# Performance work log

Measured on AMD Instinct MI355X. Metric: run time of the kernel, lower is better.

## Reference

```python
import jax, jax.numpy as jnp
import numpy as np
from jax import lax

ROPE_THETA = 10000.0


def rotate_half(x):
    d = x.shape[-1] // 2
    return jnp.concatenate([-x[..., d:], x[..., :d]], axis=-1)


def segsum(x):
    # x: (..., l) -> (..., l, l) lower-triangular segment sums (off-tri = -inf)
    T = x.shape[-1]
    cs = jnp.cumsum(x, axis=-1)
    d = cs[..., :, None] - cs[..., None, :]
    mask = jnp.tril(jnp.ones((T, T), dtype=bool))
    return jnp.where(mask, d, -jnp.inf)


def setup_inputs() -> dict:
    key = jax.random.key(0)
    ks = jax.random.split(key, 8)
    B, L, D, H = 2, 8192, 1024, 16
    P = D // H  # head_dim == state_dim
    hidden_states = jax.random.normal(ks[0], (B, L, D), dtype=jnp.float32)
    # rotary embeddings over head_dim
    inv_freq = 1.0 / (ROPE_THETA ** (np.arange(0, P, 2, dtype=np.float32) / P))
    pos = np.arange(L, dtype=np.float32)
    freqs = pos[:, None] * inv_freq[None, :]            # (L, P/2)
    emb = np.concatenate([freqs, freqs], axis=-1)       # (L, P)
    cos = jnp.asarray(np.broadcast_to(np.cos(emb), (B, L, P)).copy())
    sin = jnp.asarray(np.broadcast_to(np.sin(emb), (B, L, P)).copy())
    s = 1.0 / np.sqrt(D)
    Wc = jax.random.normal(ks[1], (D, D), dtype=jnp.float32) * s
    Wb = jax.random.normal(ks[2], (D, D), dtype=jnp.float32) * s
    Wx = jax.random.normal(ks[3], (D, D), dtype=jnp.float32) * s
    Wdt = jax.random.normal(ks[4], (D, H), dtype=jnp.float32) * s
    Wout = jax.random.normal(ks[5], (D, D), dtype=jnp.float32) * s
    # A must be negative for a stable decaying SSM (Mamba2 convention A = -exp(A_log))
    A = -(0.5 + jax.random.uniform(ks[6], (H,), dtype=jnp.float32))
    return {"hidden_states": hidden_states, "cos": cos, "sin": sin,
            "Wc": Wc, "Wb": Wb, "Wdt": Wdt, "Wx": Wx, "Wout": Wout,
            "A": A, "chunk_size": 256}


def reference(hidden_states, cos, sin, Wc, Wb, Wdt, Wx, Wout, A, chunk_size):
    B, L, D = hidden_states.shape
    H = A.shape[0]
    P = D // H
    nc = L // chunk_size
    cl = chunk_size

    c = (hidden_states @ Wc).reshape(B, L, H, P)
    b = (hidden_states @ Wb).reshape(B, L, H, P)
    x = (hidden_states @ Wx).reshape(B, L, H, P)
    dt = jax.nn.softplus(hidden_states @ Wdt)  # (B, L, H), dt_softplus=True

    # rotary on C and B (unsqueeze_dim=2)
    cosu, sinu = cos[:, :, None, :], sin[:, :, None, :]
    c = c * cosu + rotate_half(c) * sinu
    b = b * cosu + rotate_half(b) * sinu

    # chunked SSD (mamba_chunk_scan_combined)
    cr = c.reshape(B, nc, cl, H, P)
    br = b.reshape(B, nc, cl, H, P)
    xdt = (x * dt[..., None]).reshape(B, nc, cl, H, P)
    dA = (dt * A[None, None, :]).reshape(B, nc, cl, H)
    dAc = jnp.transpose(dA, (0, 3, 1, 2))            # (B, H, nc, cl)
    Acum = jnp.cumsum(dAc, axis=-1)                  # (B, H, nc, cl)

    # intra-chunk (diagonal) term
    Lmask = jnp.exp(segsum(dAc))                     # (B, H, nc, cl, cl)
    Y_diag = jnp.einsum('bclhn,bcshn,bhcls,bcshp->bclhp', cr, br, Lmask, xdt)

    # per-chunk states
    decay_states = jnp.exp(Acum[..., -1:] - Acum)    # (B, H, nc, cl)
    states = jnp.einsum('bclhn,bhcl,bclhp->bchpn', br, decay_states, xdt)
    chunk_decay = jnp.exp(Acum[..., -1])             # (B, H, nc)

    def step(h, inp):
        s, dec = inp                                 # (B,H,P,N), (B,H)
        h_new = h * dec[..., None, None] + s
        return h_new, h                              # emit state BEFORE this chunk

    states_c = jnp.moveaxis(states, 1, 0)            # (nc, B, H, P, N)
    dec_c = jnp.moveaxis(chunk_decay, 2, 0)          # (nc, B, H)
    h0 = jnp.zeros((B, H, P, P), dtype=hidden_states.dtype)
    final_state, prev_states = lax.scan(step, h0, (states_c, dec_c))
    prev_states = jnp.moveaxis(prev_states, 0, 1)    # (B, nc, H, P, N)

    # inter-chunk (off-diagonal) term
    state_decay_out = jnp.exp(Acum)                  # (B, H, nc, cl)
    Y_off = jnp.einsum('bclhn,bchpn,bhcl->bclhp', cr, prev_states, state_decay_out)

    y = (Y_diag + Y_off).reshape(B, L, D)
    out = y @ Wout
    return out, final_state
```

## Files before the change

### kernel.cpp

```cpp
#include <hip/hip_runtime.h>
#include <hip/hip_bf16.h>

typedef unsigned short u16;

#define Bb 2
#define Ll 8192
#define Dd 1024
#define Hh 16
#define Pp 64
#define CLc 256
#define NCc 32
#define Mm 16384
#define DD2 ((size_t)Dd*Dd)
#define WDTSZ ((size_t)256*1024)

typedef __attribute__((ext_vector_type(8))) short short8b;
typedef __attribute__((ext_vector_type(4))) float f32x4v;

__device__ __forceinline__ float bf2f(u16 u){
    return __uint_as_float(((unsigned int)u) << 16);
}
__device__ __forceinline__ u16 f2bf(float f){
    unsigned int i = __float_as_uint(f);
    unsigned int r = (i + 0x7FFFu + ((i >> 16) & 1u)) >> 16;
    return (u16)r;
}

template<int DT>
__device__ __forceinline__ void ld8(const void* p, size_t i, float* o){
    if (DT){
        const u16* q = (const u16*)p + i;
        ushort4 a0 = *(const ushort4*)q;
        ushort4 a1 = *(const ushort4*)(q + 4);
        o[0]=bf2f(a0.x); o[1]=bf2f(a0.y); o[2]=bf2f(a0.z); o[3]=bf2f(a0.w);
        o[4]=bf2f(a1.x); o[5]=bf2f(a1.y); o[6]=bf2f(a1.z); o[7]=bf2f(a1.w);
    } else {
        const float* q = (const float*)p + i;
        float4 a0 = *(const float4*)q;
        float4 a1 = *(const float4*)(q + 4);
        o[0]=a0.x; o[1]=a0.y; o[2]=a0.z; o[3]=a0.w;
        o[4]=a1.x; o[5]=a1.y; o[6]=a1.z; o[7]=a1.w;
    }
}
__device__ __forceinline__ float ldf(const void* p, size_t i, int dtf){
    return dtf ? bf2f(((const u16*)p)[i]) : ((const float*)p)[i];
}

typedef __attribute__((address_space(3))) void lds_t;
typedef __attribute__((address_space(1))) const void gm_t;
__device__ __forceinline__ void gload16(const void* g, void* l){
    __builtin_amdgcn_global_load_lds((gm_t*)g, (lds_t*)l, 16, 0, 0);
}

__device__ __forceinline__ void fence_barrier(){
    asm volatile("" ::: "memory");
    __builtin_amdgcn_s_barrier();
    asm volatile("" ::: "memory");
}

__global__ void sniff_kernel(const unsigned int* __restrict__ cosw, int* __restrict__ flag){
    if (threadIdx.x == 0 && blockIdx.x == 0)
        *flag = (cosw[0] == 0x3F800000u) ? 0 : 1;
}

__global__ __launch_bounds__(256) void cospack_kernel(
    const void* __restrict__ cosb, const void* __restrict__ sinb,
    float* __restrict__ cp, const int* __restrict__ flag)
{
    const int dtf = *flag;
    int i = blockIdx.x*256 + threadIdx.x;
    int tok = i >> 6, c = i & 63;
    float v = (c < 32) ? ldf(cosb, (size_t)tok*64 + c,        dtf)
                       : ldf(sinb, (size_t)tok*64 + (c - 32), dtf);
    cp[i] = v;
}

__global__ __launch_bounds__(256) void cvt_kernel(
    const void* __restrict__ in, u16* __restrict__ out, const int* __restrict__ flag)
{
    if (*flag == 1) return;
    size_t i = ((size_t)blockIdx.x*256 + threadIdx.x) * 8;
    float v[8];
    ld8<0>(in, i, v);
    ushort4 o0, o1;
    o0.x=f2bf(v[0]); o0.y=f2bf(v[1]); o0.z=f2bf(v[2]); o0.w=f2bf(v[3]);
    o1.x=f2bf(v[4]); o1.y=f2bf(v[5]); o1.z=f2bf(v[6]); o1.w=f2bf(v[7]);
    *(ushort4*)(out + i)     = o0;
    *(ushort4*)(out + i + 4) = o1;
}

__global__ __launch_bounds__(256) void wtrans_kernel(
    const void* __restrict__ W0, const void* __restrict__ W1,
    const void* __restrict__ W2, const void* __restrict__ W3,
    u16* __restrict__ out, const int* __restrict__ flag)
{
    const int dtf = *flag;
    const int z = blockIdx.z;
    const void* W = (z==0) ? W0 : (z==1) ? W1 : (z==2) ? W2 : W3;
    u16* Whi = out + (size_t)z*DD2 + (z==3 ? WDTSZ : 0);
    u16* Wlo = out + (size_t)4*DD2 + WDTSZ;
    __shared__ u16 th[64][65];
    __shared__ u16 tlo[64][65];
    const int t = threadIdx.x;
    const int r = t >> 2, cq = (t & 3)*16;
    size_t base = ((size_t)blockIdx.y*64 + r)*1024 + (size_t)blockIdx.x*64 + cq;
    float v[8];
#pragma unroll
    for (int half = 0; half < 2; half++){
        if (dtf) ld8<1>(W, base + half*8, v); else ld8<0>(W, base + half*8, v);
#pragma unroll
        for (int j = 0; j < 8; j++){
            u16 hi = f2bf(v[j]);
            th[r][cq + half*8 + j]  = hi;
            tlo[r][cq + half*8 + j] = f2bf(v[j] - bf2f(hi));
        }
    }
    __syncthreads();
    size_t ob = ((size_t)blockIdx.x*64 + r)*1024 + (size_t)blockIdx.y*64 + cq;
#pragma unroll
    for (int j = 0; j < 16; j++)
        Whi[ob + j] = th[cq + j][r];
    if (z == 3){
#pragma unroll
        for (int j = 0; j < 16; j++)
            Wlo[ob + j] = tlo[cq + j][r];
    }
}

__global__ __launch_bounds__(256) void wdtrep_kernel(
    const void* __restrict__ Wdt, u16* __restrict__ wdt, const int* __restrict__ flag)
{
    const int dtf = *flag;
    int i = blockIdx.x*256 + threadIdx.x;
    int r = i >> 10, k = i & 1023;
    wdt[i] = f2bf(ldf(Wdt, (size_t)k*16 + (r & 15), dtf));
}

template<int DTC, int ACC, int FUSE>
__global__ __launch_bounds__(512) void gemm_mfma(
    const u16* __restrict__ Abf, const void* __restrict__ Araw,
    const u16* __restrict__ Bt, void* __restrict__ C,
    int M, int N, int K, const int* __restrict__ flag, int want,
    const float* __restrict__ cp, float* __restrict__ dtb)
{
    const int dtf = *flag;
    if (want >= 0 && dtf != want) return;
    const u16* A = (FUSE && dtf) ? (const u16*)Araw : Abf;
    __shared__ __align__(128) u16 As[4][256*32];
    __shared__ __align__(128) u16 Bs[4][256*32];
    const int t    = threadIdx.x;
    const int wave = t >> 6;
    const int lane = t & 63;

    const int nbn = N >> 8;
    const int nbm = M >> 8;
    int wg = blockIdx.x, nwg = gridDim.x;
    int bm, bn;
    if ((nwg & 7) == 0 && (nbm & 7) == 0){
        const int x   = wg & 7;
        const int loc = wg >> 3;
        const int rpx = nbm >> 3;
        const int bmL = loc % rpx;
        bn = loc / rpx;
        bm = x*rpx + bmL;
    } else {
        bm = wg / nbn; bn = wg % nbn;
    }

    const int ldrow = wave*16 + (lane >> 2);
    const int ldk   = (lane & 3)*8;
    const u16* Ag0 = A  + (size_t)(bm*256 + ldrow)*K + ldk;
    const u16* Ag1 = Ag0 + (size_t)128*K;
    const u16* Bg0 = Bt + (size_t)(bn*256 + ldrow)*K + ldk;
    const u16* Bg1 = Bg0 + (size_t)128*K;
    const int o0 = (wave*16)*32;
    const int o1 = (128 + wave*16)*32;

    const int wr = wave >> 2, wc = wave & 3;
    const int fr = lane & 15;
    const int fk = (lane >> 4)*8;

    f32x4v acc[8][4] = {};

    const int steps = K >> 5;
#pragma unroll
    for (int s = 0; s < 2; s++){
        gload16(Ag0 + s*32, &As[s][o0]);
        gload16(Ag1 + s*32, &As[s][o1]);
        gload16(Bg0 + s*32, &Bs[s][o0]);
        gload16(Bg1 + s*32, &Bs[s][o1]);
    }

    for (int ts = 0; ts < steps; ++ts){
        if (ts + 2 < steps){
            const int sb = (ts + 2) & 3;
            const int ko = (ts + 2)*32;
            gload16(Ag0 + ko, &As[sb][o0]);
            gload16(Ag1 + ko, &As[sb][o1]);
            gload16(Bg0 + ko, &Bs[sb][o0]);
            gload16(Bg1 + ko, &Bs[sb][o1]);
            asm volatile("s_waitcnt vmcnt(8)" ::: "memory");
        } else if (ts + 1 < steps){
            asm volatile("s_waitcnt vmcnt(4)" ::: "memory");
        } else {
            asm volatile("s_waitcnt vmcnt(0)" ::: "memory");
        }
        fence_barrier();
        const int cb = ts & 3;
        const u16* a_rd = &As[cb][(wr*128 + fr)*32 + fk];
        const u16* b_rd = &Bs[cb][(wc*64 + fr)*32 + fk];
        short8b af[8], bfv[4];
#pragma unroll
        for (int i = 0; i < 8; i++)
            af[i]  = *(const short8b*)(a_rd + i*16*32);
#pragma unroll
        for (int i = 0; i < 4; i++)
            bfv[i] = *(const short8b*)(b_rd + i*16*32);
#pragma unroll
        for (int mi = 0; mi < 8; mi++)
#pragma unroll
            for (int ni = 0; ni < 4; ni++)
                acc[mi][ni] = __builtin_amdgcn_mfma_f32_16x16x32_bf16(
                    af[mi], bfv[ni], acc[mi][ni], 0, 0, 0);
    }

    const int crow = (lane >> 4)*4;
    const int ccol = lane & 15;

    if (FUSE && bn == nbn - 1){
        if (wc == 0){
#pragma unroll
            for (int mi = 0; mi < 8; mi++){
#pragma unroll
                for (int r = 0; r < 4; r++){
                    size_t row = (size_t)bm*256 + wr*128 + mi*16 + crow + r;
                    float v = acc[mi][0][r];
                    float sp = (v > 20.f) ? v : log1pf(__expf(v));
                    dtb[row*16 + ccol] = sp;
                }
            }
        }
        return;
    }

    const int bufid = FUSE ? (bn >> 2) : 0;
    const int bnl   = FUSE ? (bn & 3) : bn;
    u16* Cf = FUSE ? ((u16*)C + (size_t)bufid*((size_t)Mm*Dd)) : (u16*)C;
    const size_t Nout = FUSE ? (size_t)Dd : (size_t)N;

    if (FUSE && bufid < 2){
#pragma unroll
        for (int mi = 0; mi < 8; mi++){
#pragma unroll
            for (int r = 0; r < 4; r++){
                size_t row = (size_t)bm*256 + wr*128 + mi*16 + crow + r;
                const float* cpr = cp + (size_t)(row & (Ll-1))*64;
                float cs0 = cpr[ccol],      cs1 = cpr[ccol + 16];
                float sn0 = cpr[32 + ccol], sn1 = cpr[48 + ccol];
                float a0 = acc[mi][0][r], a1 = acc[mi][1][r];
                float a2 = acc[mi][2][r], a3 = acc[mi][3][r];
                acc[mi][0][r] = a0*cs0 - a2*sn0;
                acc[mi][2][r] = a2*cs0 + a0*sn0;
                acc[mi][1][r] = a1*cs1 - a3*sn1;
                acc[mi][3][r] = a3*cs1 + a1*sn1;
            }
        }
    }

#pragma unroll
    for (int mi = 0; mi < 8; mi++){
#pragma unroll
        for (int ni = 0; ni < 4; ni++){
            size_t col = (size_t)bnl*256 + wc*64 + ni*16 + ccol;
#pragma unroll
            for (int r = 0; r < 4; r++){
                size_t row = (size_t)bm*256 + wr*128 + mi*16 + crow + r;
                float v = acc[mi][ni][r];
                if (DTC){
                    Cf[row*Nout + col] = f2bf(v);
                } else {
                    float* p = (float*)C + row*Nout + col;
                    *p = ACC ? (*p + v) : v;
                }
            }
        }
    }
}

__global__ __launch_bounds__(512) void chunk_kernel(
    const u16* __restrict__ cr, u16* brY, const u16* __restrict__ xd,
    float* __restrict__ Acum, float* __restrict__ states,
    const float* __restrict__ dtb, const void* __restrict__ Aarr,
    const int* __restrict__ flag)
{
    __shared__ u16 brs[256*72];
    __shared__ u16 brTs[64*264];
    __shared__ u16 xdsT[64*264];
    __shared__ u16 plds[8][32*72];
    __shared__ float acs[256];
    __shared__ float wexp[256];
    const int dtf = *flag;
    const int g = blockIdx.x;
    const int h = g & 15, c = (g >> 4) & 31, b = g >> 9;
    const int t = threadIdx.x;
    const int w = t >> 6, lane = t & 63;
    const size_t tokbase = (size_t)b*Ll + (size_t)c*CLc;
    float* Acw = Acum + ((size_t)(b*Hh + h)*NCc + c)*CLc;

    if (t < 256)
        acs[t] = dtb[(tokbase + t)*Hh + h] * ldf(Aarr, h, dtf);
    __syncthreads();
    for (int off = 1; off < 256; off <<= 1){
        float add = (t < 256 && t >= off) ? acs[t - off] : 0.f;
        __syncthreads();
        if (t < 256) acs[t] += add;
        __syncthreads();
    }
    const float a_last = acs[255];
    if (t < 256){
        wexp[t] = __expf(fminf(a_last - acs[t], 0.f));
        Acw[t] = acs[t];
    }
    __syncthreads();

#pragma unroll
    for (int i = 0; i < 4; i++){
        int f8 = i*512 + t;
        int l  = f8 >> 3;
        int n8 = (f8 & 7)*8;
        size_t goff = (tokbase + l)*Dd + h*Pp + n8;
        ushort4 a0 = *(const ushort4*)&brY[goff];
        ushort4 a1 = *(const ushort4*)&brY[goff + 4];
        *(ushort4*)&brs[l*72 + n8]     = a0;
        *(ushort4*)&brs[l*72 + n8 + 4] = a1;
        float wl = wexp[l];
        u16 bv[8] = {(u16)a0.x,(u16)a0.y,(u16)a0.z,(u16)a0.w,
                     (u16)a1.x,(u16)a1.y,(u16)a1.z,(u16)a1.w};
#pragma unroll
        for (int j = 0; j < 8; j++)
            brTs[(n8 + j)*264 + l] = f2bf(wl * bf2f(bv[j]));
        float dl = dtb[(tokbase + l)*Hh + h];
        ushort4 x0 = *(const ushort4*)&xd[goff];
        ushort4 x1 = *(const ushort4*)&xd[goff + 4];
        u16 xv[8] = {(u16)x0.x,(u16)x0.y,(u16)x0.z,(u16)x0.w,
                     (u16)x1.x,(u16)x1.y,(u16)x1.z,(u16)x1.w};
#pragma unroll
        for (int j = 0; j < 8; j++)
            xdsT[(n8 + j)*264 + l] = f2bf(bf2f(xv[j]) * dl);
    }
    __syncthreads();

    const int fr = lane & 15;
    const int kb = (lane >> 4)*8;

    {
        int ks0 = 0;
        for (int ks = 0; ks < 8; ks++){
            if (a_last - acs[ks*32 + 31] >= -30.f){ ks0 = ks; break; }
        }
        const int pi  = w >> 1;
        const int ni0 = (w & 1)*2;
        f32x4v sacc[2] = {};
        const int pr = pi*16 + fr;
        for (int ks = ks0; ks < 8; ks++){
            short8b afr = *(const short8b*)&xdsT[pr*264 + ks*32 + kb];
#pragma unroll
            for (int q = 0; q < 2; q++){
                short8b bfr = *(const short8b*)&brTs[((ni0+q)*16 + fr)*264 + ks*32 + kb];
                sacc[q] = __builtin_amdgcn_mfma_f32_16x16x32_bf16(afr, bfr, sacc[q], 0, 0, 0);
            }
        }
        float* st = states + ((size_t)((b*NCc + c)*Hh) + h)*4096;
        const int prow = pi*16 + (lane >> 4)*4;
#pragma unroll
        for (int q = 0; q < 2; q++)
#pragma unroll
            for (int r = 0; r < 4; r++)
                st[(prow + r)*64 + (ni0+q)*16 + fr] = sacc[q][r];
    }

    {
        short8b crf[2][2];
#pragma unroll
        for (int mi = 0; mi < 2; mi++)
#pragma unroll
            for (int ks = 0; ks < 2; ks++)
                crf[mi][ks] = *(const short8b*)&cr[(tokbase + w*32 + mi*16 + fr)*Dd + h*Pp + ks*32 + kb];

        float al[2][4];
#pragma unroll
        for (int mi = 0; mi < 2; mi++)
#pragma unroll
            for (int r = 0; r < 4; r++)
                al[mi][r] = acs[w*32 + mi*16 + (lane >> 4)*4 + r];

        f32x4v yacc[2][4] = {};
        u16* pw = &plds[w][0];
        const float a_hi = acs[w*32];

        for (int cb = w >> 1; cb >= 0; --cb){
            if (a_hi - acs[cb*64 + 63] < -30.f) break;
#pragma unroll
            for (int mi = 0; mi < 2; mi++){
#pragma unroll
                for (int ni = 0; ni < 4; ni++){
                    f32x4v s4 = {};
#pragma unroll
                    for (int ks = 0; ks < 2; ks++){
                        short8b bfr = *(const short8b*)&brs[(cb*64 + ni*16 + fr)*72 + ks*32 + kb];
                        s4 = __builtin_amdgcn_mfma_f32_16x16x32_bf16(crf[mi][ks], bfr, s4, 0, 0, 0);
                    }
                    const int s_idx = cb*64 + ni*16 + fr;
                    const float a_s = acs[s_idx];
                    const int lrow0 = w*32 + mi*16 + (lane >> 4)*4;
#pragma unroll
                    for (int r = 0; r < 4; r++){
                        float wgt = __expf(fminf(al[mi][r] - a_s, 0.f));
                        float pv  = (s_idx <= lrow0 + r) ? wgt * s4[r] : 0.f;
                        pw[(mi*16 + (lane >> 4)*4 + r)*72 + ni*16 + fr] = f2bf(pv);
                    }
                }
            }
            asm volatile("s_waitcnt lgkmcnt(0)" ::: "memory");
#pragma unroll
            for (int ks = 0; ks < 2; ks++){
                short8b paf[2];
#pragma unroll
                for (int mi = 0; mi < 2; mi++)
                    paf[mi] = *(const short8b*)&pw[(mi*16 + fr)*72 + ks*32 + kb];
#pragma unroll
                for (int pi = 0; pi < 4; pi++){
                    short8b xbf = *(const short8b*)&xdsT[(pi*16 + fr)*264 + cb*64 + ks*32 + kb];
#pragma unroll
                    for (int mi = 0; mi < 2; mi++)
                        yacc[mi][pi] = __builtin_amdgcn_mfma_f32_16x16x32_bf16(paf[mi], xbf, yacc[mi][pi], 0, 0, 0);
                }
            }
        }
#pragma unroll
        for (int mi = 0; mi < 2; mi++){
            const int lrow = w*32 + mi*16 + (lane >> 4)*4;
#pragma unroll
            for (int r = 0; r < 4; r++){
                u16* yp = brY + (tokbase + lrow + r)*Dd + h*Pp + fr;
#pragma unroll
                for (int pi = 0; pi < 4; pi++)
                    yp[pi*16] = f2bf(yacc[mi][pi][r]);
            }
        }
    }
}

__global__ __launch_bounds__(256) void scan_kernel(
    float* st, const float* __restrict__ Acum, void* d_out, const int* __restrict__ flag)
{
    const int dtf = *flag;
    const int g = blockIdx.x;
    const int seg = g & 15;
    const int bh = g >> 4;
    const int h = bh & 15, b = bh >> 4;
    const int e = seg*256 + threadIdx.x;
    const float* Ac = Acum + (size_t)(b*Hh + h)*NCc*CLc;
    float hst = 0.f;
    for (int c = 0; c < NCc; c++){
        float dec = __expf(fminf(Ac[c*CLc + 255], 0.f));
        size_t off = ((size_t)((b*NCc + c)*Hh) + h)*4096 + e;
        float s_val = st[off];
        st[off] = hst;
        hst = hst*dec + s_val;
    }
    size_t fi = (size_t)Mm*Dd + (size_t)(b*Hh + h)*4096 + e;
    if (dtf) ((u16*)d_out)[fi] = f2bf(hst);
    else     ((float*)d_out)[fi] = hst;
}

__global__ __launch_bounds__(256) void yoff_kernel(
    const u16* __restrict__ cr, const float* __restrict__ prev,
    const float* __restrict__ Acum, u16* y)
{
    __shared__ u16 pvb[64*72];
    __shared__ float acs[256];
    const int g = blockIdx.x;
    const int h = g & 15, c = (g >> 4) & 31, b = g >> 9;
    const int t = threadIdx.x;
    const int wv = t >> 6, lane = t & 63;
    const size_t tokbase = (size_t)b*Ll + (size_t)c*CLc;
    const float* pv = prev + ((size_t)((b*NCc + c)*Hh) + h)*4096;
    const float* Ac = Acum + ((size_t)(b*Hh + h)*NCc + c)*CLc;
    acs[t] = Ac[t];
#pragma unroll
    for (int i = 0; i < 16; i++){
        int f = i*256 + t;
        int p = f >> 6, n = f & 63;
        pvb[p*72 + n] = f2bf(pv[f]);
    }
    __syncthreads();

    const int fr = lane & 15;
    const int kb = (lane >> 4)*8;

    short8b crf[4][2];
#pragma unroll
    for (int mi = 0; mi < 4; mi++)
#pragma unroll
        for (int ks = 0; ks < 2; ks++)
            crf[mi][ks] = *(const short8b*)&cr[(tokbase + wv*64 + mi*16 + fr)*Dd + h*Pp + ks*32 + kb];

    f32x4v yacc[4][4] = {};
#pragma unroll
    for (int ks = 0; ks < 2; ks++){
        short8b pbf[4];
#pragma unroll
        for (int pi = 0; pi < 4; pi++)
            pbf[pi] = *(const short8b*)&pvb[(pi*16 + fr)*72 + ks*32 + kb];
#pragma unroll
        for (int mi = 0; mi < 4; mi++)
#pragma unroll
            for (int pi = 0; pi < 4; pi++)
                yacc[mi][pi] = __builtin_amdgcn_mfma_f32_16x16x32_bf16(
                    crf[mi][ks], pbf[pi], yacc[mi][pi], 0, 0, 0);
    }

    const int crw = (lane >> 4)*4;
#pragma unroll
    for (int mi = 0; mi < 4; mi++){
        const int lrow = wv*64 + mi*16 + crw;
#pragma unroll
        for (int r = 0; r < 4; r++){
            float el = __expf(fminf(acs[lrow + r], 0.f));
            u16* yp = y + (tokbase + lrow + r)*Dd + h*Pp + fr;
#pragma unroll
            for (int pi = 0; pi < 4; pi++){
                float cur = bf2f(yp[pi*16]);
                yp[pi*16] = f2bf(cur + el*yacc[mi][pi][r]);
            }
        }
    }
}

__global__ __launch_bounds__(256) void zero_out_kernel(void* o, long long n, const int* flag)
{
    long long i = (long long)blockIdx.x*256 + threadIdx.x;
    if (i < n){
        if (*flag) ((u16*)o)[i] = 0;
        else       ((float*)o)[i] = 0.f;
    }
}

extern "C" void kernel_launch(void* const* d_in, const int* in_sizes, int n_in,
                              void* d_out, int out_size, void* d_ws, size_t ws_size,
                              hipStream_t stream)
{
    const void* hs   = d_in[0];
    const void* cosb = d_in[1];
    const void* sinb = d_in[2];
    const void* Wc   = d_in[3];
    const void* Wb   = d_in[4];
    const void* Wdt  = d_in[5];
    const void* Wx   = d_in[6];
    const void* Wout = d_in[7];
    const void* Aarr = d_in[8];

    int*  flag  = (int*)d_ws;
    char* wbase = (char*)d_ws + 1024;

    const size_t NEED = 1024
                      + (size_t)3*Mm*Dd*2
                      + (size_t)Mm*Hh*4
                      + (size_t)Bb*Hh*Ll*4
                      + (size_t)Bb*NCc*Hh*4096*4
                      + (size_t)Mm*Dd*2
                      + ((size_t)5*DD2 + WDTSZ)*2
                      + (size_t)Ll*64*4;

    sniff_kernel<<<1, 64, 0, stream>>>((const unsigned int*)cosb, flag);

    if (ws_size < NEED){
        long long n = (long long)out_size;
        zero_out_kernel<<<(unsigned)((n + 255)/256), 256, 0, stream>>>(d_out, n, flag);
        return;
    }

    u16*   c_buf  = (u16*)wbase;
    u16*   b_buf  = c_buf + (size_t)Mm*Dd;
    u16*   x_buf  = b_buf + (size_t)Mm*Dd;
    float* dt_buf = (float*)(x_buf + (size_t)Mm*Dd);
    float* acum   = dt_buf + (size_t)Mm*Hh;
    float* states = acum + (size_t)Bb*Hh*Ll;
    u16*   hs_bf  = (u16*)(states + (size_t)Bb*NCc*Hh*4096);
    u16*   wt     = hs_bf + (size_t)Mm*Dd;
    float* cp     = (float*)(wt + (size_t)5*DD2 + WDTSZ);

    cvt_kernel<<<(Mm*Dd)/(256*8), 256, 0, stream>>>(hs, hs_bf, flag);
    wtrans_kernel<<<dim3(16,16,4), 256, 0, stream>>>(Wc, Wb, Wx, Wout, wt, flag);
    wdtrep_kernel<<<(256*1024)/256, 256, 0, stream>>>(Wdt, wt + 3*DD2, flag);
    cospack_kernel<<<(Ll*64)/256, 256, 0, stream>>>(cosb, sinb, cp, flag);

    gemm_mfma<1,0,1><<<(Mm/256)*(3328/256), 512, 0, stream>>>(
        hs_bf, hs, wt, c_buf, Mm, 3328, Dd, flag, -1, cp, dt_buf);

    chunk_kernel<<<Bb*NCc*Hh, 512, 0, stream>>>(c_buf, b_buf, x_buf, acum, states, dt_buf, Aarr, flag);
    scan_kernel<<<Bb*Hh*16, 256, 0, stream>>>(states, acum, d_out, flag);
    yoff_kernel<<<Bb*NCc*Hh, 256, 0, stream>>>(c_buf, states, acum, b_buf);

    const int NWG = (Mm/256)*(Dd/256);
    u16* woutT = wt + 3*DD2 + WDTSZ;
    u16* woutL = wt + 4*DD2 + WDTSZ;
    gemm_mfma<1,0,0><<<NWG, 512, 0, stream>>>(b_buf, nullptr, woutT, d_out, Mm, Dd, Dd, flag, 1, nullptr, nullptr);
    gemm_mfma<0,0,0><<<NWG, 512, 0, stream>>>(b_buf, nullptr, woutT, d_out, Mm, Dd, Dd, flag, 0, nullptr, nullptr);
    gemm_mfma<0,1,0><<<NWG, 512, 0, stream>>>(b_buf, nullptr, woutL, d_out, Mm, Dd, Dd, flag, 0, nullptr, nullptr);
}
```

Baseline: 478.7 us.

## Shrink GEMM tiles to 128x128 with 256 threads and double buffering

Replaces the 256x256-tile, 512-thread GEMM with a 128x128-tile, 256-thread version. The four-stage LDS ring with explicit vmcnt waits becomes a two-buffer scheme synchronised by __syncthreads. The fused projection GEMM now uses N=3200, with the dt columns in a single 128-wide tile. Smaller tiles give more workgroups and less LDS per block, in exchange for lower operand reuse and shallower prefetch that exposes more global-load latency.

```diff
diff --git a/kernel.cpp b/kernel.cpp
--- a/kernel.cpp
+++ b/kernel.cpp
@@ -52,12 +52,6 @@
     __builtin_amdgcn_global_load_lds((gm_t*)g, (lds_t*)l, 16, 0, 0);
 }
 
-__device__ __forceinline__ void fence_barrier(){
-    asm volatile("" ::: "memory");
-    __builtin_amdgcn_s_barrier();
-    asm volatile("" ::: "memory");
-}
-
 __global__ void sniff_kernel(const unsigned int* __restrict__ cosw, int* __restrict__ flag){
     if (threadIdx.x == 0 && blockIdx.x == 0)
         *flag = (cosw[0] == 0x3F800000u) ? 0 : 1;
@@ -137,7 +131,7 @@
 }
 
 template<int DTC, int ACC, int FUSE>
-__global__ __launch_bounds__(512) void gemm_mfma(
+__global__ __launch_bounds__(256) void gemm_mfma(
     const u16* __restrict__ Abf, const void* __restrict__ Araw,
     const u16* __restrict__ Bt, void* __restrict__ C,
     int M, int N, int K, const int* __restrict__ flag, int want,
@@ -146,14 +140,14 @@
     const int dtf = *flag;
     if (want >= 0 && dtf != want) return;
     const u16* A = (FUSE && dtf) ? (const u16*)Araw : Abf;
-    __shared__ __align__(128) u16 As[4][256*32];
-    __shared__ __align__(128) u16 Bs[4][256*32];
+    __shared__ __align__(128) u16 As[2][128*32];
+    __shared__ __align__(128) u16 Bs[2][128*32];
     const int t    = threadIdx.x;
     const int wave = t >> 6;
     const int lane = t & 63;
 
-    const int nbn = N >> 8;
-    const int nbm = M >> 8;
+    const int nbn = N >> 7;
+    const int nbm = M >> 7;
     int wg = blockIdx.x, nwg = gridDim.x;
     int bm, bn;
     if ((nwg & 7) == 0 && (nbm & 7) == 0){
@@ -169,59 +163,51 @@
 
     const int ldrow = wave*16 + (lane >> 2);
     const int ldk   = (lane & 3)*8;
-    const u16* Ag0 = A  + (size_t)(bm*256 + ldrow)*K + ldk;
-    const u16* Ag1 = Ag0 + (size_t)128*K;
-    const u16* Bg0 = Bt + (size_t)(bn*256 + ldrow)*K + ldk;
-    const u16* Bg1 = Bg0 + (size_t)128*K;
+    const u16* Ag0 = A  + (size_t)(bm*128 + ldrow)*K + ldk;
+    const u16* Ag1 = Ag0 + (size_t)64*K;
+    const u16* Bg0 = Bt + (size_t)(bn*128 + ldrow)*K + ldk;
+    const u16* Bg1 = Bg0 + (size_t)64*K;
     const int o0 = (wave*16)*32;
-    const int o1 = (128 + wave*16)*32;
-
-    const int wr = wave >> 2, wc = wave & 3;
+    const int o1 = (64 + wave*16)*32;
+
+    const int wr = wave >> 1, wc = wave & 1;
     const int fr = lane & 15;
     const int fk = (lane >> 4)*8;
 
-    f32x4v acc[8][4] = {};
+    f32x4v acc[4][4] = {};
 
     const int steps = K >> 5;
-#pragma unroll
-    for (int s = 0; s < 2; s++){
-        gload16(Ag0 + s*32, &As[s][o0]);
-        gload16(Ag1 + s*32, &As[s][o1]);
-        gload16(Bg0 + s*32, &Bs[s][o0]);
-        gload16(Bg1 + s*32, &Bs[s][o1]);
-    }
+    gload16(Ag0, &As[0][o0]);
+    gload16(Ag1, &As[0][o1]);
+    gload16(Bg0, &Bs[0][o0]);
+    gload16(Bg1, &Bs[0][o1]);
+    __syncthreads();
 
     for (int ts = 0; ts < steps; ++ts){
-        if (ts + 2 < steps){
-            const int sb = (ts + 2) & 3;
-            const int ko = (ts + 2)*32;
-            gload16(Ag0 + ko, &As[sb][o0]);
-            gload16(Ag1 + ko, &As[sb][o1]);
-            gload16(Bg0 + ko, &Bs[sb][o0]);
-            gload16(Bg1 + ko, &Bs[sb][o1]);
-            asm volatile("s_waitcnt vmcnt(8)" ::: "memory");
-        } else if (ts + 1 < steps){
-            asm volatile("s_waitcnt vmcnt(4)" ::: "memory");
-        } else {
-            asm volatile("s_waitcnt vmcnt(0)" ::: "memory");
-        }
-        fence_barrier();
-        const int cb = ts & 3;
-        const u16* a_rd = &As[cb][(wr*128 + fr)*32 + fk];
-        const u16* b_rd = &Bs[cb][(wc*64 + fr)*32 + fk];
-        short8b af[8], bfv[4];
-#pragma unroll
-        for (int i = 0; i < 8; i++)
+        const int cur = ts & 1;
+        if (ts + 1 < steps){
+            const int nb = cur ^ 1;
+            const int ko = (ts + 1)*32;
+            gload16(Ag0 + ko, &As[nb][o0]);
+            gload16(Ag1 + ko, &As[nb][o1]);
+            gload16(Bg0 + ko, &Bs[nb][o0]);
+            gload16(Bg1 + ko, &Bs[nb][o1]);
+        }
+        const u16* a_rd = &As[cur][(wr*64 + fr)*32 + fk];
+        const u16* b_rd = &Bs[cur][(wc*64 + fr)*32 + fk];
+        short8b af[4], bfv[4];
+#pragma unroll
+        for (int i = 0; i < 4; i++){
             af[i]  = *(const short8b*)(a_rd + i*16*32);
-#pragma unroll
-        for (int i = 0; i < 4; i++)
             bfv[i] = *(const short8b*)(b_rd + i*16*32);
-#pragma unroll
-        for (int mi = 0; mi < 8; mi++)
+        }
+#pragma unroll
+        for (int mi = 0; mi < 4; mi++)
 #pragma unroll
             for (int ni = 0; ni < 4; ni++)
                 acc[mi][ni] = __builtin_amdgcn_mfma_f32_16x16x32_bf16(
                     af[mi], bfv[ni], acc[mi][ni], 0, 0, 0);
+        __syncthreads();
     }
 
     const int crow = (lane >> 4)*4;
@@ -230,10 +216,10 @@
     if (FUSE && bn == nbn - 1){
         if (wc == 0){
 #pragma unroll
-            for (int mi = 0; mi < 8; mi++){
+            for (int mi = 0; mi < 4; mi++){
 #pragma unroll
                 for (int r = 0; r < 4; r++){
-                    size_t row = (size_t)bm*256 + wr*128 + mi*16 + crow + r;
+                    size_t row = (size_t)bm*128 + wr*64 + mi*16 + crow + r;
                     float v = acc[mi][0][r];
                     float sp = (v > 20.f) ? v : log1pf(__expf(v));
                     dtb[row*16 + ccol] = sp;
@@ -243,17 +229,17 @@
         return;
     }
 
-    const int bufid = FUSE ? (bn >> 2) : 0;
-    const int bnl   = FUSE ? (bn & 3) : bn;
+    const int bufid = FUSE ? (bn >> 3) : 0;
+    const int bnl   = FUSE ? (bn & 7) : bn;
     u16* Cf = FUSE ? ((u16*)C + (size_t)bufid*((size_t)Mm*Dd)) : (u16*)C;
     const size_t Nout = FUSE ? (size_t)Dd : (size_t)N;
 
     if (FUSE && bufid < 2){
 #pragma unroll
-        for (int mi = 0; mi < 8; mi++){
+        for (int mi = 0; mi < 4; mi++){
 #pragma unroll
             for (int r = 0; r < 4; r++){
-                size_t row = (size_t)bm*256 + wr*128 + mi*16 + crow + r;
+                size_t row = (size_t)bm*128 + wr*64 + mi*16 + crow + r;
                 const float* cpr = cp + (size_t)(row & (Ll-1))*64;
                 float cs0 = cpr[ccol],      cs1 = cpr[ccol + 16];
                 float sn0 = cpr[32 + ccol], sn1 = cpr[48 + ccol];
@@ -268,13 +254,13 @@
     }
 
 #pragma unroll
-    for (int mi = 0; mi < 8; mi++){
+    for (int mi = 0; mi < 4; mi++){
 #pragma unroll
         for (int ni = 0; ni < 4; ni++){
-            size_t col = (size_t)bnl*256 + wc*64 + ni*16 + ccol;
+            size_t col = (size_t)bnl*128 + wc*64 + ni*16 + ccol;
 #pragma unroll
             for (int r = 0; r < 4; r++){
-                size_t row = (size_t)bm*256 + wr*128 + mi*16 + crow + r;
+                size_t row = (size_t)bm*128 + wr*64 + mi*16 + crow + r;
                 float v = acc[mi][ni][r];
                 if (DTC){
                     Cf[row*Nout + col] = f2bf(v);
@@ -596,17 +582,17 @@
     wdtrep_kernel<<<(256*1024)/256, 256, 0, stream>>>(Wdt, wt + 3*DD2, flag);
     cospack_kernel<<<(Ll*64)/256, 256, 0, stream>>>(cosb, sinb, cp, flag);
 
-    gemm_mfma<1,0,1><<<(Mm/256)*(3328/256), 512, 0, stream>>>(
-        hs_bf, hs, wt, c_buf, Mm, 3328, Dd, flag, -1, cp, dt_buf);
+    gemm_mfma<1,0,1><<<(Mm/128)*(3200/128), 256, 0, stream>>>(
+        hs_bf, hs, wt, c_buf, Mm, 3200, Dd, flag, -1, cp, dt_buf);
 
     chunk_kernel<<<Bb*NCc*Hh, 512, 0, stream>>>(c_buf, b_buf, x_buf, acum, states, dt_buf, Aarr, flag);
     scan_kernel<<<Bb*Hh*16, 256, 0, stream>>>(states, acum, d_out, flag);
     yoff_kernel<<<Bb*NCc*Hh, 256, 0, stream>>>(c_buf, states, acum, b_buf);
 
-    const int NWG = (Mm/256)*(Dd/256);
+    const int NWG = (Mm/128)*(Dd/128);
     u16* woutT = wt + 3*DD2 + WDTSZ;
     u16* woutL = wt + 4*DD2 + WDTSZ;
-    gemm_mfma<1,0,0><<<NWG, 512, 0, stream>>>(b_buf, nullptr, woutT, d_out, Mm, Dd, Dd, flag, 1, nullptr, nullptr);
-    gemm_mfma<0,0,0><<<NWG, 512, 0, stream>>>(b_buf, nullptr, woutT, d_out, Mm, Dd, Dd, flag, 0, nullptr, nullptr);
-    gemm_mfma<0,1,0><<<NWG, 512, 0, stream>>>(b_buf, nullptr, woutL, d_out, Mm, Dd, Dd, flag, 0, nullptr, nullptr);
-}
+    gemm_mfma<1,0,0><<<NWG, 256, 0, stream>>>(b_buf, nullptr, woutT, d_out, Mm, Dd, Dd, flag, 1, nullptr, nullptr);
+    gemm_mfma<0,0,0><<<NWG, 256, 0, stream>>>(b_buf, nullptr, woutT, d_out, Mm, Dd, Dd, flag, 0, nullptr, nullptr);
+    gemm_mfma<0,1,0><<<NWG, 256, 0, stream>>>(b_buf, nullptr, woutL, d_out, Mm, Dd, Dd, flag, 0, nullptr, nullptr);
+}
```

After: 518.2 us. 8.3% more time.
